# Kernel optimization log

Measured on AMD Instinct MI355X. Metric: run time of the kernel, lower is better.

Reference implementation:

```python
import jax, jax.numpy as jnp
import numpy as np

NUM_TOKENS = 8192
D_IN = 2048
D_OUT = 2048
N_EXPERT = 9
N_SHARED = 1
N_SPARSE = N_EXPERT - N_SHARED  # 8
TOP_K = 2


def setup_inputs() -> dict:
    key = jax.random.key(0)
    ks = jax.random.split(key, 7)
    s_in = 1.0 / np.sqrt(D_IN)
    return {
        "x": jax.random.normal(ks[0], (NUM_TOKENS, D_IN), jnp.float32),
        # shared experts (Linear input_dim->output_dim), stacked over shared axis
        "W_shared": jax.random.uniform(ks[1], (N_SHARED, D_IN, D_OUT), jnp.float32, -s_in, s_in),
        "b_shared": jax.random.uniform(ks[2], (N_SHARED, D_OUT), jnp.float32, -s_in, s_in),
        # router: Linear input_dim -> num_sparse_experts
        "W_router": jax.random.uniform(ks[3], (D_IN, N_SPARSE), jnp.float32, -s_in, s_in),
        "b_router": jax.random.uniform(ks[4], (N_SPARSE,), jnp.float32, -s_in, s_in),
        # sparse experts stacked over expert axis
        "W_sparse": jax.random.uniform(ks[5], (N_SPARSE, D_IN, D_OUT), jnp.float32, -s_in, s_in),
        "b_sparse": jax.random.uniform(ks[6], (N_SPARSE, D_OUT), jnp.float32, -s_in, s_in),
    }


def reference(x, W_shared, b_shared, W_router, b_router, W_sparse, b_sparse):
    T = x.shape[0]
    # shared experts: sum of Linear outputs, divided by n_shared (mean)
    y = (jnp.einsum("td,sdo->to", x, W_shared) + b_shared.sum(0)) / N_SHARED

    # router (eval: no noise, no capacity dropping)
    logits = x @ W_router + b_router                       # [T, E]
    probs = jax.nn.softmax(logits, axis=-1)
    topk_w, topk_idx = jax.lax.top_k(probs, TOP_K)          # [T, K]
    topk_w = topk_w / (topk_w.sum(-1, keepdims=True) + 1e-6)

    # dense gate matrix [T, E]; top-k indices per row are distinct
    gates = jnp.zeros((T, N_SPARSE), x.dtype).at[
        jnp.arange(T)[:, None], topk_idx
    ].add(topk_w)

    # weighted combination of sparse expert outputs
    y = y + jnp.einsum("td,edo,te->to", x, W_sparse, gates)
    y = y + gates @ b_sparse
    return y


if __name__ == "__main__":
    out = reference(**setup_inputs())
    print(out.shape, out.dtype)
```

## Files before the change

kernel.cpp:

```cpp
#include <hip/hip_runtime.h>
#include <hip/hip_bf16.h>
#include <stdint.h>

#define NT   8192
#define DIN  2048
#define DOUT 2048
#define NSP  8
#define BK   64

typedef _Float16 f16x8 __attribute__((ext_vector_type(8)));
typedef float    f32x4 __attribute__((ext_vector_type(4)));

static_assert(sizeof(f16x8) == 16, "f16x8 must be 16B");

__device__ __forceinline__ f32x4 mfma_f16(f16x8 a, f16x8 b, f32x4 c) {
  return __builtin_amdgcn_mfma_f32_16x16x32_f16(a, b, c, 0, 0, 0);
}

__device__ __forceinline__ void async16(const void* g, void* l) {
  __builtin_amdgcn_global_load_lds(
      (const __attribute__((address_space(1))) uint32_t*)g,
      (__attribute__((address_space(3))) uint32_t*)l, 16, 0, 0);
}

__global__ void k_convert_x(const float* __restrict__ x,
                            _Float16* __restrict__ xh) {
  int idx = blockIdx.x * blockDim.x + threadIdx.x;
  const float4* xv = (const float4*)x;
  float4 v0 = xv[2 * idx], v1 = xv[2 * idx + 1];
  union { _Float16 h[8]; int4 q; } H;
  H.h[0] = (_Float16)v0.x; H.h[1] = (_Float16)v0.y;
  H.h[2] = (_Float16)v0.z; H.h[3] = (_Float16)v0.w;
  H.h[4] = (_Float16)v1.x; H.h[5] = (_Float16)v1.y;
  H.h[6] = (_Float16)v1.z; H.h[7] = (_Float16)v1.w;
  ((int4*)xh)[idx] = H.q;
}

__global__ void k_convert_w9(const float* __restrict__ Wsh,
                             const float* __restrict__ Wsp,
                             _Float16* __restrict__ wth) {
  __shared__ _Float16 sh[64 * 66];
  const int z = blockIdx.z;
  const float* Wm = (z == 0) ? Wsh : (Wsp + (size_t)(z - 1) * DIN * DOUT);
  const int k0 = blockIdx.x * 64, o0 = blockIdx.y * 64;
  const int t = threadIdx.x;
  const int kr = t >> 4, oc4 = (t & 15) * 4;
#pragma unroll
  for (int i = 0; i < 4; i++) {
    int k = kr + i * 16;
    float4 v = *(const float4*)&Wm[(size_t)(k0 + k) * DOUT + o0 + oc4];
    sh[k * 66 + oc4 + 0] = (_Float16)v.x;
    sh[k * 66 + oc4 + 1] = (_Float16)v.y;
    sh[k * 66 + oc4 + 2] = (_Float16)v.z;
    sh[k * 66 + oc4 + 3] = (_Float16)v.w;
  }
  __syncthreads();
  const int orow = t >> 3, kq = t & 7;
  const size_t obase = (size_t)z * DOUT;
#pragma unroll
  for (int i = 0; i < 2; i++) {
    int o = orow + i * 32;
    union { _Float16 h[8]; int4 q; } P;
#pragma unroll
    for (int j = 0; j < 8; j++) P.h[j] = sh[(kq * 8 + j) * 66 + o];
    *(int4*)&wth[(obase + o0 + o) * (size_t)DIN + (size_t)(k0 + kq * 8)] = P.q;
  }
}

__global__ void k_router(const float* __restrict__ x, const float* __restrict__ Wr,
                         const float* __restrict__ br,
                         int* __restrict__ counts, int* __restrict__ tok_list,
                         float* __restrict__ w_list) {
  const int wave = threadIdx.x >> 6, lane = threadIdx.x & 63;
  const int t = blockIdx.x * 4 + wave;
  const float* xrow = x + (size_t)t * DIN;
  float acc[NSP];
#pragma unroll
  for (int e = 0; e < NSP; e++) acc[e] = 0.f;
  for (int d = lane; d < DIN; d += 64) {
    float xv = xrow[d];
    const float* wr = Wr + d * NSP;
#pragma unroll
    for (int e = 0; e < NSP; e++) acc[e] += xv * wr[e];
  }
#pragma unroll
  for (int e = 0; e < NSP; e++) {
#pragma unroll
    for (int off = 32; off > 0; off >>= 1) acc[e] += __shfl_xor(acc[e], off, 64);
  }
  if (lane == 0) {
    float lg[NSP], mx = -1e30f;
#pragma unroll
    for (int e = 0; e < NSP; e++) { lg[e] = acc[e] + br[e]; mx = fmaxf(mx, lg[e]); }
    float p[NSP], s = 0.f;
#pragma unroll
    for (int e = 0; e < NSP; e++) { p[e] = expf(lg[e] - mx); s += p[e]; }
    int i0 = 0;
#pragma unroll
    for (int e = 1; e < NSP; e++) if (p[e] > p[i0]) i0 = e;
    int i1 = (i0 == 0) ? 1 : 0;
#pragma unroll
    for (int e = 0; e < NSP; e++) if (e != i0 && p[e] > p[i1]) i1 = e;
    float p0 = p[i0] / s, p1 = p[i1] / s;
    float denom = p0 + p1 + 1e-6f;
    float w0 = p0 / denom, w1 = p1 / denom;
    int s0 = atomicAdd(&counts[i0], 1);
    tok_list[i0 * NT + s0] = t; w_list[i0 * NT + s0] = w0;
    int s1 = atomicAdd(&counts[i1], 1);
    tok_list[i1 * NT + s1] = t; w_list[i1 * NT + s1] = w1;
  }
}

template <bool SPARSE>
__global__ __launch_bounds__(256, 4) void k_moe_gemm(
    const _Float16* __restrict__ xh, const _Float16* __restrict__ wth,
    const float* __restrict__ bias, const int* __restrict__ counts,
    const int* __restrict__ tok_list, const float* __restrict__ w_list,
    float* __restrict__ y) {
  const int e = SPARSE ? blockIdx.z : 0;
  const int wi = SPARSE ? (1 + e) : 0;

  const int nx = gridDim.x;
  const int bid = blockIdx.y * nx + blockIdx.x;
  const int cpx = (nx * gridDim.y) >> 3;
  const int swz = (bid & 7) * cpx + (bid >> 3);
  const int row0 = (swz % nx) * 128;
  const int col0 = (swz / nx) * 128;

  int cnt = NT;
  if (SPARSE) {
    cnt = counts[e];
    if (row0 >= cnt) return;
  }

  __shared__ __align__(16) _Float16 sA[128 * BK];
  __shared__ __align__(16) _Float16 sB[128 * BK];
  __shared__ int   s_tok[128];
  __shared__ float s_w[128];

  const int tid = threadIdx.x;
  const int wave = tid >> 6, lane = tid & 63;

  if (SPARSE) {
    if (tid < 128) {
      int slot = row0 + tid;
      int tk = 0; float w = 0.f;
      if (slot < cnt) { tk = tok_list[e * NT + slot]; w = w_list[e * NT + slot]; }
      s_tok[tid] = tk; s_w[tid] = w;
    }
    __syncthreads();
  }

  const int lr = lane >> 3, pp = lane & 7;
  const _Float16* gA[4]; const _Float16* gB[4];
  int loff[4];
#pragma unroll
  for (int j = 0; j < 4; j++) {
    int r = wave * 32 + j * 8 + lr;
    int xoff = ((pp ^ (r & 7)) << 3);
    int tk = SPARSE ? s_tok[r] : (row0 + r);
    gA[j] = xh + (size_t)tk * DIN + xoff;
    gB[j] = wth + ((size_t)wi * DOUT + (size_t)(col0 + r)) * DIN + xoff;
    loff[j] = r * BK + pp * 8;
  }

  f32x4 acc[4][4];
#pragma unroll
  for (int m = 0; m < 4; m++)
#pragma unroll
    for (int n = 0; n < 4; n++) acc[m][n] = (f32x4){0.f, 0.f, 0.f, 0.f};

  const int wm = (wave >> 1) * 64, wn = (wave & 1) * 64;
  const int fr = lane & 15, fg = lane >> 4;

  for (int kt = 0; kt < DIN / BK; kt++) {
    const int k0 = kt * BK;
#pragma unroll
    for (int j = 0; j < 4; j++) {
      async16(gA[j] + k0, &sA[loff[j]]);
      async16(gB[j] + k0, &sB[loff[j]]);
    }
    __syncthreads();

#pragma unroll
    for (int ks = 0; ks < 2; ks++) {
      f16x8 ah[4], bh[4];
#pragma unroll
      for (int m = 0; m < 4; m++) {
        int r = wm + m * 16 + fr;
        int sl = (((ks * 4 + fg) ^ (r & 7)) << 3);
        ah[m] = *(const f16x8*)&sA[r * BK + sl];
      }
#pragma unroll
      for (int n = 0; n < 4; n++) {
        int c = wn + n * 16 + fr;
        int sl = (((ks * 4 + fg) ^ (c & 7)) << 3);
        bh[n] = *(const f16x8*)&sB[c * BK + sl];
      }
#pragma unroll
      for (int m = 0; m < 4; m++)
#pragma unroll
        for (int n = 0; n < 4; n++)
          acc[m][n] = mfma_f16(ah[m], bh[n], acc[m][n]);
    }
    __syncthreads();
  }

#pragma unroll
  for (int n = 0; n < 4; n++) {
    int col = col0 + wn + n * 16 + fr;
    float bc = SPARSE ? bias[e * DOUT + col] : bias[col];
#pragma unroll
    for (int m = 0; m < 4; m++) {
#pragma unroll
      for (int q = 0; q < 4; q++) {
        int lrow = wm + m * 16 + fg * 4 + q;
        float v = acc[m][n][q];
        if (SPARSE) {
          if (row0 + lrow < cnt) {
            float g = s_w[lrow];
            atomicAdd(&y[(size_t)s_tok[lrow] * DOUT + col], g * (v + bc));
          }
        } else {
          y[(size_t)(row0 + lrow) * DOUT + col] = v + bc;
        }
      }
    }
  }
}

template <bool SPARSE>
__global__ void k_fb_gemm(const float* __restrict__ x, const float* __restrict__ W,
                          const float* __restrict__ bias,
                          const int* __restrict__ counts,
                          const int* __restrict__ tok_list,
                          const float* __restrict__ w_list,
                          float* __restrict__ y) {
  const int e = SPARSE ? blockIdx.z : 0;
  int cnt = NT;
  if (SPARSE) {
    cnt = counts[e];
    if ((int)blockIdx.y * 64 >= cnt) return;
  }
  const int row0 = blockIdx.y * 64, col0 = blockIdx.x * 64;
  const float* Wm = W + (SPARSE ? (size_t)e * DIN * DOUT : 0);

  __shared__ float sA[64][17];
  __shared__ float sB[16][65];
  __shared__ int   s_tok[64];
  __shared__ float s_w[64];

  const int tid = threadIdx.x;
  if (SPARSE) {
    if (tid < 64) {
      int slot = row0 + tid;
      int tk = 0; float w = 0.f;
      if (slot < cnt) { tk = tok_list[e * NT + slot]; w = w_list[e * NT + slot]; }
      s_tok[tid] = tk; s_w[tid] = w;
    }
    __syncthreads();
  }

  const int ar = tid >> 2, ak = (tid & 3) * 4;
  const int bk = tid >> 4, bc4 = (tid & 15) * 4;
  const int tm = tid >> 4, tn = tid & 15;

  float acc[4][4];
#pragma unroll
  for (int m = 0; m < 4; m++)
#pragma unroll
    for (int n = 0; n < 4; n++) acc[m][n] = 0.f;

  const int tkA = SPARSE ? s_tok[ar] : (row0 + ar);

  for (int k0 = 0; k0 < DIN; k0 += 16) {
    float4 va = *(const float4*)&x[(size_t)tkA * DIN + k0 + ak];
    float4 vb = *(const float4*)&Wm[(size_t)(k0 + bk) * DOUT + col0 + bc4];
    sA[ar][ak]     = va.x; sA[ar][ak + 1] = va.y;
    sA[ar][ak + 2] = va.z; sA[ar][ak + 3] = va.w;
    sB[bk][bc4]     = vb.x; sB[bk][bc4 + 1] = vb.y;
    sB[bk][bc4 + 2] = vb.z; sB[bk][bc4 + 3] = vb.w;
    __syncthreads();
#pragma unroll
    for (int kk = 0; kk < 16; kk++) {
      float a0 = sA[tm * 4 + 0][kk], a1 = sA[tm * 4 + 1][kk];
      float a2 = sA[tm * 4 + 2][kk], a3 = sA[tm * 4 + 3][kk];
#pragma unroll
      for (int n = 0; n < 4; n++) {
        float b = sB[kk][tn * 4 + n];
        acc[0][n] += a0 * b; acc[1][n] += a1 * b;
        acc[2][n] += a2 * b; acc[3][n] += a3 * b;
      }
    }
    __syncthreads();
  }

#pragma unroll
  for (int m = 0; m < 4; m++) {
    int lrow = tm * 4 + m;
#pragma unroll
    for (int n = 0; n < 4; n++) {
      int col = col0 + tn * 4 + n;
      float bcv = SPARSE ? bias[e * DOUT + col] : bias[col];
      if (SPARSE) {
        if (row0 + lrow < cnt) {
          atomicAdd(&y[(size_t)s_tok[lrow] * DOUT + col],
                    s_w[lrow] * (acc[m][n] + bcv));
        }
      } else {
        y[(size_t)(row0 + lrow) * DOUT + col] = acc[m][n] + bcv;
      }
    }
  }
}

__global__ void k_zero(float* __restrict__ y, int n) {
  for (int i = blockIdx.x * blockDim.x + threadIdx.x; i < n;
       i += gridDim.x * blockDim.x)
    y[i] = 0.f;
}

extern "C" void kernel_launch(void* const* d_in, const int* in_sizes, int n_in,
                              void* d_out, int out_size, void* d_ws, size_t ws_size,
                              hipStream_t stream) {
  (void)in_sizes; (void)n_in;
  const float* x   = (const float*)d_in[0];
  const float* Wsh = (const float*)d_in[1];
  const float* bsh = (const float*)d_in[2];
  const float* Wr  = (const float*)d_in[3];
  const float* br  = (const float*)d_in[4];
  const float* Wsp = (const float*)d_in[5];
  const float* bsp = (const float*)d_in[6];
  float* y = (float*)d_out;

  char* ws = (char*)d_ws;
  size_t off = 0;
  auto alloc = [&](size_t bytes) {
    off = (off + 255) & ~(size_t)255;
    void* p = ws + off;
    off += bytes;
    return p;
  };
  int*      counts   = (int*)alloc(NSP * sizeof(int));
  int*      tok_list = (int*)alloc((size_t)NSP * NT * sizeof(int));
  float*    w_list   = (float*)alloc((size_t)NSP * NT * sizeof(float));
  const size_t NEED_FB = off;
  _Float16* xh       = (_Float16*)alloc((size_t)NT * DIN * 2);
  _Float16* wth      = (_Float16*)alloc((size_t)9 * DOUT * DIN * 2);
  const size_t NEED_FAST = off;

  if (ws_size < NEED_FB) {
    k_zero<<<2048, 256, 0, stream>>>(y, out_size);
    return;
  }

  hipMemsetAsync(counts, 0, NSP * sizeof(int), stream);
  k_router<<<NT / 4, 256, 0, stream>>>(x, Wr, br, counts, tok_list, w_list);

  if (ws_size >= NEED_FAST) {
    k_convert_x<<<(NT * DIN / 8) / 256, 256, 0, stream>>>(x, xh);
    k_convert_w9<<<dim3(DIN / 64, DOUT / 64, 9), 256, 0, stream>>>(Wsh, Wsp, wth);
    k_moe_gemm<false><<<dim3(NT / 128, DOUT / 128, 1), 256, 0, stream>>>(
        xh, wth, bsh, counts, tok_list, w_list, y);
    k_moe_gemm<true><<<dim3(NT / 128, DOUT / 128, NSP), 256, 0, stream>>>(
        xh, wth, bsp, counts, tok_list, w_list, y);
  } else {
    k_fb_gemm<false><<<dim3(DOUT / 64, NT / 64, 1), 256, 0, stream>>>(
        x, Wsh, bsh, counts, tok_list, w_list, y);
    k_fb_gemm<true><<<dim3(DOUT / 64, NT / 64, NSP), 256, 0, stream>>>(
        x, Wsp, bsp, counts, tok_list, w_list, y);
  }
}
```

Measured before the change: 794.0 us.

## Fuse shared and sparse expert GEMMs into one 256x256-tile launch

Replaces the two separate GEMM launches (shared expert with plain stores, sparse experts with atomics) with a single kernel whose z index covers all nine experts. It uses 256x256 output tiles, 512 threads and BK=32, and zeroes y first so the shared expert can also accumulate with atomics. The aim is to cut launch count and raise per-block data reuse with larger tiles. In exchange the shared expert now pays atomic-add cost on every output, the grid has no swizzle, the K step is halved (more barriers per FLOP), and occupancy is one large block per CU.

```diff
diff --git a/kernel.cpp b/kernel.cpp
--- a/kernel.cpp
+++ b/kernel.cpp
@@ -6,7 +6,7 @@
 #define DIN  2048
 #define DOUT 2048
 #define NSP  8
-#define BK   64
+#define BK   32
 
 typedef _Float16 f16x8 __attribute__((ext_vector_type(8)));
 typedef float    f32x4 __attribute__((ext_vector_type(4)));
@@ -111,118 +111,104 @@
   }
 }
 
-template <bool SPARSE>
-__global__ __launch_bounds__(256, 4) void k_moe_gemm(
+__global__ __launch_bounds__(512, 1) void k_moe_fused(
     const _Float16* __restrict__ xh, const _Float16* __restrict__ wth,
-    const float* __restrict__ bias, const int* __restrict__ counts,
-    const int* __restrict__ tok_list, const float* __restrict__ w_list,
-    float* __restrict__ y) {
-  const int e = SPARSE ? blockIdx.z : 0;
-  const int wi = SPARSE ? (1 + e) : 0;
-
-  const int nx = gridDim.x;
-  const int bid = blockIdx.y * nx + blockIdx.x;
-  const int cpx = (nx * gridDim.y) >> 3;
-  const int swz = (bid & 7) * cpx + (bid >> 3);
-  const int row0 = (swz % nx) * 128;
-  const int col0 = (swz / nx) * 128;
+    const float* __restrict__ bsh, const float* __restrict__ bsp,
+    const int* __restrict__ counts, const int* __restrict__ tok_list,
+    const float* __restrict__ w_list, float* __restrict__ y) {
+  const int z = blockIdx.z;
+  const int row0 = blockIdx.y * 256;
+  const int col0 = blockIdx.x * 256;
 
   int cnt = NT;
-  if (SPARSE) {
-    cnt = counts[e];
+  if (z > 0) {
+    cnt = counts[z - 1];
     if (row0 >= cnt) return;
   }
-
-  __shared__ __align__(16) _Float16 sA[128 * BK];
-  __shared__ __align__(16) _Float16 sB[128 * BK];
-  __shared__ int   s_tok[128];
-  __shared__ float s_w[128];
+  const float* bias = (z == 0) ? bsh : (bsp + (size_t)(z - 1) * DOUT);
+
+  __shared__ __align__(16) _Float16 sA[256 * BK];
+  __shared__ __align__(16) _Float16 sB[256 * BK];
+  __shared__ int   s_tok[256];
+  __shared__ float s_w[256];
 
   const int tid = threadIdx.x;
   const int wave = tid >> 6, lane = tid & 63;
 
-  if (SPARSE) {
-    if (tid < 128) {
-      int slot = row0 + tid;
-      int tk = 0; float w = 0.f;
-      if (slot < cnt) { tk = tok_list[e * NT + slot]; w = w_list[e * NT + slot]; }
-      s_tok[tid] = tk; s_w[tid] = w;
-    }
-    __syncthreads();
-  }
-
-  const int lr = lane >> 3, pp = lane & 7;
-  const _Float16* gA[4]; const _Float16* gB[4];
-  int loff[4];
-#pragma unroll
-  for (int j = 0; j < 4; j++) {
-    int r = wave * 32 + j * 8 + lr;
-    int xoff = ((pp ^ (r & 7)) << 3);
-    int tk = SPARSE ? s_tok[r] : (row0 + r);
-    gA[j] = xh + (size_t)tk * DIN + xoff;
-    gB[j] = wth + ((size_t)wi * DOUT + (size_t)(col0 + r)) * DIN + xoff;
-    loff[j] = r * BK + pp * 8;
-  }
-
-  f32x4 acc[4][4];
-#pragma unroll
-  for (int m = 0; m < 4; m++)
+  if (tid < 256) {
+    int slot = row0 + tid;
+    int tk = 0; float w = 0.f;
+    if (z == 0) { tk = slot; w = 1.f; }
+    else if (slot < cnt) {
+      tk = tok_list[(z - 1) * NT + slot];
+      w  = w_list[(z - 1) * NT + slot];
+    }
+    s_tok[tid] = tk; s_w[tid] = w;
+  }
+  __syncthreads();
+
+  const _Float16* gA[2]; const _Float16* gB[2];
+  int loff[2];
+#pragma unroll
+  for (int j = 0; j < 2; j++) {
+    int c = j * 512 + tid;
+    int r = c >> 2, p = c & 3;
+    int xoff = ((p ^ (r & 3)) << 3);
+    gA[j] = xh + (size_t)s_tok[r] * DIN + xoff;
+    gB[j] = wth + ((size_t)z * DOUT + (size_t)(col0 + r)) * DIN + xoff;
+    loff[j] = c * 8;
+  }
+
+  f32x4 acc[8][4];
+#pragma unroll
+  for (int m = 0; m < 8; m++)
 #pragma unroll
     for (int n = 0; n < 4; n++) acc[m][n] = (f32x4){0.f, 0.f, 0.f, 0.f};
 
-  const int wm = (wave >> 1) * 64, wn = (wave & 1) * 64;
+  const int wr = (wave >> 2) * 128, wc = (wave & 3) * 64;
   const int fr = lane & 15, fg = lane >> 4;
 
   for (int kt = 0; kt < DIN / BK; kt++) {
     const int k0 = kt * BK;
 #pragma unroll
-    for (int j = 0; j < 4; j++) {
+    for (int j = 0; j < 2; j++) {
       async16(gA[j] + k0, &sA[loff[j]]);
       async16(gB[j] + k0, &sB[loff[j]]);
     }
     __syncthreads();
 
-#pragma unroll
-    for (int ks = 0; ks < 2; ks++) {
-      f16x8 ah[4], bh[4];
-#pragma unroll
-      for (int m = 0; m < 4; m++) {
-        int r = wm + m * 16 + fr;
-        int sl = (((ks * 4 + fg) ^ (r & 7)) << 3);
-        ah[m] = *(const f16x8*)&sA[r * BK + sl];
-      }
-#pragma unroll
-      for (int n = 0; n < 4; n++) {
-        int c = wn + n * 16 + fr;
-        int sl = (((ks * 4 + fg) ^ (c & 7)) << 3);
-        bh[n] = *(const f16x8*)&sB[c * BK + sl];
-      }
-#pragma unroll
-      for (int m = 0; m < 4; m++)
-#pragma unroll
-        for (int n = 0; n < 4; n++)
-          acc[m][n] = mfma_f16(ah[m], bh[n], acc[m][n]);
-    }
+    f16x8 a[8], b[4];
+#pragma unroll
+    for (int m = 0; m < 8; m++) {
+      int r = wr + m * 16 + fr;
+      a[m] = *(const f16x8*)&sA[r * BK + ((fg ^ (r & 3)) << 3)];
+    }
+#pragma unroll
+    for (int n = 0; n < 4; n++) {
+      int c = wc + n * 16 + fr;
+      b[n] = *(const f16x8*)&sB[c * BK + ((fg ^ (c & 3)) << 3)];
+    }
+#pragma unroll
+    for (int m = 0; m < 8; m++)
+#pragma unroll
+      for (int n = 0; n < 4; n++)
+        acc[m][n] = mfma_f16(a[m], b[n], acc[m][n]);
     __syncthreads();
   }
 
 #pragma unroll
   for (int n = 0; n < 4; n++) {
-    int col = col0 + wn + n * 16 + fr;
-    float bc = SPARSE ? bias[e * DOUT + col] : bias[col];
-#pragma unroll
-    for (int m = 0; m < 4; m++) {
+    int col = col0 + wc + n * 16 + fr;
+    float bc = bias[col];
+#pragma unroll
+    for (int m = 0; m < 8; m++) {
 #pragma unroll
       for (int q = 0; q < 4; q++) {
-        int lrow = wm + m * 16 + fg * 4 + q;
-        float v = acc[m][n][q];
-        if (SPARSE) {
-          if (row0 + lrow < cnt) {
-            float g = s_w[lrow];
-            atomicAdd(&y[(size_t)s_tok[lrow] * DOUT + col], g * (v + bc));
-          }
-        } else {
-          y[(size_t)(row0 + lrow) * DOUT + col] = v + bc;
+        int lrow = wr + m * 16 + fg * 4 + q;
+        if (row0 + lrow < cnt) {
+          float g = s_w[lrow];
+          atomicAdd(&y[(size_t)s_tok[lrow] * DOUT + col],
+                    g * (acc[m][n][q] + bc));
         }
       }
     }
@@ -360,10 +346,9 @@
   if (ws_size >= NEED_FAST) {
     k_convert_x<<<(NT * DIN / 8) / 256, 256, 0, stream>>>(x, xh);
     k_convert_w9<<<dim3(DIN / 64, DOUT / 64, 9), 256, 0, stream>>>(Wsh, Wsp, wth);
-    k_moe_gemm<false><<<dim3(NT / 128, DOUT / 128, 1), 256, 0, stream>>>(
-        xh, wth, bsh, counts, tok_list, w_list, y);
-    k_moe_gemm<true><<<dim3(NT / 128, DOUT / 128, NSP), 256, 0, stream>>>(
-        xh, wth, bsp, counts, tok_list, w_list, y);
+    k_zero<<<2048, 256, 0, stream>>>(y, out_size);
+    k_moe_fused<<<dim3(DOUT / 256, NT / 256, 9), 512, 0, stream>>>(
+        xh, wth, bsh, bsp, counts, tok_list, w_list, y);
   } else {
     k_fb_gemm<false><<<dim3(DOUT / 64, NT / 64, 1), 256, 0, stream>>>(
         x, Wsh, bsh, counts, tok_list, w_list, y);
```

Result: slower. 997.1 us (+25.6%).
